# Kernel optimization log

Hardware: AMD Instinct MI355X
Metric: run time of the kernel (lower is better)

## Reference

```python
import jax, jax.numpy as jnp
import numpy as np

B, LV, LS = 16, 512, 512
FEA_V, FEA_S = 2048, 768
D_MODEL, H, DK, DV = 1024, 16, 64, 64
EPS = 1e-6


def setup_inputs() -> dict:
    key = jax.random.key(0)
    ks = jax.random.split(key, 16)
    sc = lambda fan_in: 1.0 / np.sqrt(fan_in)
    return {
        "v": jax.random.normal(ks[0], (B, LV, FEA_V), jnp.float32),
        "s": jax.random.normal(ks[1], (B, LS, FEA_S), jnp.float32),
        "W_lv": jax.random.normal(ks[2], (FEA_V, D_MODEL), jnp.float32) * sc(FEA_V),
        "b_lv": jnp.zeros((D_MODEL,), jnp.float32),
        "W_ls": jax.random.normal(ks[3], (FEA_S, D_MODEL), jnp.float32) * sc(FEA_S),
        "b_ls": jnp.zeros((D_MODEL,), jnp.float32),
        "pos_v": jax.random.normal(ks[4], (1, LV, D_MODEL), jnp.float32),
        "pos_s": jax.random.normal(ks[5], (1, LS, D_MODEL), jnp.float32),
        "W_q": jax.random.normal(ks[6], (D_MODEL, H * DK), jnp.float32) * sc(D_MODEL),
        "b_q": jnp.zeros((H * DK,), jnp.float32),
        "W_k": jax.random.normal(ks[7], (D_MODEL, H * DK), jnp.float32) * sc(D_MODEL),
        "b_k": jnp.zeros((H * DK,), jnp.float32),
        "W_v": jax.random.normal(ks[8], (D_MODEL, H * DV), jnp.float32) * sc(D_MODEL),
        "b_v": jnp.zeros((H * DV,), jnp.float32),
        "W_p": jax.random.normal(ks[9], (H * DV, D_MODEL), jnp.float32) * sc(H * DV),
        "b_p": jnp.zeros((D_MODEL,), jnp.float32),
        "ln_gamma": jnp.ones((D_MODEL,), jnp.float32),
        "ln_beta": jnp.zeros((D_MODEL,), jnp.float32),
        "v_len": LV,
        "s_len": LS,
    }


def _layer_norm(x, gamma, beta):
    mu = jnp.mean(x, axis=-1, keepdims=True)
    var = jnp.var(x, axis=-1, keepdims=True)
    return gamma * (x - mu) / jnp.sqrt(var + EPS) + beta


def reference(v, s, W_lv, b_lv, W_ls, b_ls, pos_v, pos_s, W_q, b_q, W_k, b_k,
              W_v, b_v, W_p, b_p, ln_gamma, ln_beta, v_len, s_len):
    b_size = v.shape[0]
    # input projections + ReLU (dropout is identity at eval)
    v = jax.nn.relu(v @ W_lv + b_lv)  # [B, LV, D]
    s = jax.nn.relu(s @ W_ls + b_ls)  # [B, LS, D]
    # positional embedding add (pos=True)
    residual_v = v + pos_v[:, : v.shape[1], :]
    # QKV projections; note the original unpack `q_v, k_s, k_s = ...`
    # overwrites the key with the VALUE projection of s, so both key and
    # value in attention are v_s (the W_v projection of s). W_k output is
    # computed in torch but discarded.
    q = (v @ W_q + b_q).reshape(b_size, -1, H, DK).transpose(0, 2, 1, 3)   # [B,H,LV,DK]
    _k = (s @ W_k + b_k)  # computed then discarded, kept for faithfulness
    vs = (s @ W_v + b_v).reshape(b_size, -1, H, DV).transpose(0, 2, 1, 3)  # [B,H,LS,DV]
    scores = jnp.einsum("bhqd,bhkd->bhqk", q, vs) / jnp.sqrt(jnp.float32(DK))
    attn = jax.nn.softmax(scores, axis=-1)
    context = jnp.einsum("bhqk,bhkd->bhqd", attn, vs)  # [B,H,LV,DV]
    context = context.transpose(0, 2, 1, 3).reshape(b_size, -1, H * DV)
    output_v = context @ W_p + b_p  # dropout identity at eval
    return _layer_norm(residual_v + output_v, ln_gamma, ln_beta)
```

## Files before the change

kernel.cpp:

```cpp
#include <hip/hip_runtime.h>

typedef unsigned short u16;
typedef unsigned int   u32;

using bf16x8 = __attribute__((ext_vector_type(8))) short;
using f32x4  = __attribute__((ext_vector_type(4))) float;

#define MFMA16(a, b, c) __builtin_amdgcn_mfma_f32_16x16x32_bf16((a), (b), (c), 0, 0, 0)

__device__ __forceinline__ u16 f2bf(float f) {
  union { float f; u32 u; } x; x.f = f;
  u32 r = x.u + 0x7fffu + ((x.u >> 16) & 1u);
  return (u16)(r >> 16);
}

__device__ __forceinline__ float bf2f(u16 v) {
  union { u32 u; float f; } x; x.u = ((u32)v) << 16;
  return x.f;
}

__device__ __forceinline__ u32 cvtpk(float lo, float hi) {
  u32 r;
  asm("v_cvt_pk_bf16_f32 %0, %1, %2" : "=v"(r) : "v"(lo), "v"(hi));
  return r;
}

__device__ __forceinline__ void gl2lds16(const void* g, void* l) {
  __builtin_amdgcn_global_load_lds(
      (const __attribute__((address_space(1))) u32*)g,
      (__attribute__((address_space(3))) u32*)l, 16, 0, 0);
}

__global__ __launch_bounds__(256) void cvt_f32_bf16(const float* __restrict__ in,
                                                    u16* __restrict__ out, long n8) {
  long i = (long)blockIdx.x * 256 + threadIdx.x;
  if (i >= n8) return;
  const float4* p = (const float4*)(in + i * 8);
  float4 a = p[0], b = p[1];
  uint4 pk;
  pk.x = cvtpk(a.x, a.y);
  pk.y = cvtpk(a.z, a.w);
  pk.z = cvtpk(b.x, b.y);
  pk.w = cvtpk(b.z, b.w);
  *(uint4*)(out + i * 8) = pk;
}

__global__ __launch_bounds__(256) void wt_cvt_t(const float* __restrict__ W,
                                                u16* __restrict__ Wt, int K, int N) {
  __shared__ u16 t[64][66];
  int tilesN = N >> 6;
  int k0 = ((int)blockIdx.x / tilesN) << 6;
  int n0 = ((int)blockIdx.x % tilesN) << 6;
  int tid = threadIdx.x;
  int c4 = (tid & 15) * 4, r16 = tid >> 4;
#pragma unroll
  for (int p = 0; p < 4; ++p) {
    int row = r16 + p * 16;
    float4 f = *(const float4*)(W + (size_t)(k0 + row) * N + n0 + c4);
    t[row][c4 + 0] = f2bf(f.x);
    t[row][c4 + 1] = f2bf(f.y);
    t[row][c4 + 2] = f2bf(f.z);
    t[row][c4 + 3] = f2bf(f.w);
  }
  __syncthreads();
  int c8 = (tid & 7) * 8, r32 = tid >> 3;
#pragma unroll
  for (int p = 0; p < 2; ++p) {
    int n = r32 + p * 32;
    u16 tmp[8] __attribute__((aligned(16)));
#pragma unroll
    for (int e = 0; e < 8; ++e) tmp[e] = t[c8 + e][n];
    *(uint4*)(Wt + (size_t)(n0 + n) * K + k0 + c8) = *(uint4*)tmp;
  }
}

template <int MODE>
__global__ __launch_bounds__(512) void gemm_bf16(
    const u16* __restrict__ A, const u16* __restrict__ Bt,
    const float* __restrict__ bias, u16* __restrict__ outb, float* __restrict__ outf,
    u16* __restrict__ outt, const u16* __restrict__ add0b,
    const float* __restrict__ add1, int M, int N, int K) {
  __shared__ u16 sA[2][128 * 64];
  __shared__ u16 sB[2][128 * 64];
  int tilesN = N >> 7;
  int nwg = (int)gridDim.x;
  int cpx = nwg >> 3;
  int orig = (int)blockIdx.x;
  int wg = (orig & 7) * cpx + (orig >> 3);
  int tm = wg / tilesN, tn = wg % tilesN;
  int m0 = tm << 7, n0 = tn << 7;
  int tid = threadIdx.x, w = tid >> 6, l = tid & 63;
  int wm = (w >> 2) << 6, wn = (w & 3) << 5;
  int c16 = l & 15, hi = l >> 4, g16 = hi * 16;

  f32x4 acc[4][2];
#pragma unroll
  for (int i = 0; i < 4; ++i)
#pragma unroll
    for (int j = 0; j < 2; ++j) acc[i][j] = (f32x4){0.f, 0.f, 0.f, 0.f};

  auto STAGE = [&](int kt, int buf) {
    const u16* Ab = A + (size_t)m0 * K + kt * 64;
    const u16* Bb = Bt + (size_t)n0 * K + kt * 64;
#pragma unroll
    for (int p = 0; p < 2; ++p) {
      int lin = p * 8192 + tid * 16;
      int row = lin >> 7;
      int cb = (lin & 127) ^ ((row & 7) << 4);
      int base = lin & ~1023;
      gl2lds16(Ab + (size_t)row * K + (cb >> 1), (char*)sA[buf] + base);
      gl2lds16(Bb + (size_t)row * K + (cb >> 1), (char*)sB[buf] + base);
    }
  };

  auto COMPUTE = [&](int buf) {
#pragma unroll
    for (int kk = 0; kk < 2; ++kk) {
      bf16x8 af[4], bfr[2];
#pragma unroll
      for (int i = 0; i < 4; ++i) {
        int ar = wm + i * 16 + c16;
        af[i] = *(const bf16x8*)((const char*)sA[buf] + ar * 128 +
                                 ((kk * 64 + g16) ^ ((ar & 7) << 4)));
      }
#pragma unroll
      for (int j = 0; j < 2; ++j) {
        int br = wn + j * 16 + c16;
        bfr[j] = *(const bf16x8*)((const char*)sB[buf] + br * 128 +
                                  ((kk * 64 + g16) ^ ((br & 7) << 4)));
      }
#pragma unroll
      for (int i = 0; i < 4; ++i)
#pragma unroll
        for (int j = 0; j < 2; ++j) acc[i][j] = MFMA16(bfr[j], af[i], acc[i][j]);
    }
  };

  int nk = K >> 6;
  STAGE(0, 0);
  int cur = 0;
  for (int kt = 0; kt < nk; ++kt) {
    if (kt + 1 < nk) {
      STAGE(kt + 1, cur ^ 1);
      __builtin_amdgcn_sched_barrier(0);
      asm volatile("s_waitcnt vmcnt(4)" ::: "memory");
    } else {
      asm volatile("s_waitcnt vmcnt(0)" ::: "memory");
    }
    __builtin_amdgcn_s_barrier();
    __builtin_amdgcn_sched_barrier(0);
    COMPUTE(cur);
    __builtin_amdgcn_sched_barrier(0);
    __builtin_amdgcn_s_barrier();
    cur ^= 1;
  }

#pragma unroll
  for (int i = 0; i < 4; ++i) {
    int gm = m0 + wm + i * 16 + c16;
#pragma unroll
    for (int j = 0; j < 2; ++j) {
      int gn0 = n0 + wn + j * 16 + hi * 4;
      float4 b4 = *(const float4*)(bias + gn0);
      float vv[4];
      vv[0] = acc[i][j][0] + b4.x;
      vv[1] = acc[i][j][1] + b4.y;
      vv[2] = acc[i][j][2] + b4.z;
      vv[3] = acc[i][j][3] + b4.w;
      if (MODE == 0) {
#pragma unroll
        for (int r = 0; r < 4; ++r) vv[r] = fmaxf(vv[r], 0.f);
        uint2 pw;
        pw.x = cvtpk(vv[0], vv[1]);
        pw.y = cvtpk(vv[2], vv[3]);
        *(uint2*)(outb + (size_t)gm * N + gn0) = pw;
      } else if (MODE == 2 || MODE == 4) {
        int hh = gn0 >> 6, dk0 = gn0 & 63, bb2 = gm >> 9, ll2 = gm & 511;
        uint2 pw;
        pw.x = cvtpk(vv[0], vv[1]);
        pw.y = cvtpk(vv[2], vv[3]);
        *(uint2*)(outb + (((size_t)bb2 * 16 + hh) * 512 + ll2) * 64 + dk0) = pw;
        if (MODE == 4) {
          u16* tb = outt + ((size_t)bb2 * 16 + hh) * 32768 + ll2;
#pragma unroll
          for (int r = 0; r < 4; ++r) tb[(size_t)(dk0 + r) * 512] = f2bf(vv[r]);
        }
      } else {
        uint2 a0 = *(const uint2*)(add0b + (size_t)gm * N + gn0);
        float4 a1 = *(const float4*)(add1 + (size_t)(gm & 511) * N + gn0);
        float4 o;
        o.x = vv[0] + bf2f((u16)(a0.x & 0xffff)) + a1.x;
        o.y = vv[1] + bf2f((u16)(a0.x >> 16)) + a1.y;
        o.z = vv[2] + bf2f((u16)(a0.y & 0xffff)) + a1.z;
        o.w = vv[3] + bf2f((u16)(a0.y >> 16)) + a1.w;
        *(float4*)(outf + (size_t)gm * N + gn0) = o;
      }
    }
  }
}

__global__ __launch_bounds__(512) void attn_kernel(const u16* __restrict__ q,
                                                   const u16* __restrict__ kv,
                                                   const u16* __restrict__ kvT,
                                                   u16* __restrict__ ctx) {
  __shared__ u16 sK[2][4096];
  __shared__ u16 sVT[2][4096];
  __shared__ u16 sP[8192];

  int orig = (int)blockIdx.x;
  int r = (orig & 7) * 128 + (orig >> 3);
  int bh = r >> 2, qt = r & 3;
  int b = bh >> 4, h = bh & 15;
  int tid = threadIdx.x, w = tid >> 6, l = tid & 63;
  int c16 = l & 15, hi = l >> 4, g16 = hi * 16;
  int swzq = (c16 & 7) << 4;

  const u16* qbase = q + (size_t)bh * 32768 + (size_t)qt * 8192;
#pragma unroll
  for (int j = 0; j < 2; ++j) {
    int chunk = w * 2 + j;
    int lin = chunk * 1024 + l * 16;
    int row = lin >> 7;
    int cb = (lin & 127) ^ ((row & 7) << 4);
    gl2lds16(qbase + (size_t)row * 64 + (cb >> 1), (char*)sP + chunk * 1024);
  }
  {
    const u16* kb = kv + (size_t)bh * 32768;
    const u16* vb = kvT + (size_t)bh * 32768;
    int lin = w * 1024 + l * 16;
    int row = lin >> 7;
    int cb = (lin & 127) ^ ((row & 7) << 4);
    gl2lds16(kb + (size_t)row * 64 + (cb >> 1), (char*)sK[0] + w * 1024);
    gl2lds16(vb + (size_t)row * 512 + (cb >> 1), (char*)sVT[0] + w * 1024);
  }
  __syncthreads();

  const char* sQrow = (const char*)sP + (w * 16 + c16) * 128;
  bf16x8 qf0 = *(const bf16x8*)(sQrow + ((0 + g16) ^ swzq));
  bf16x8 qf1 = *(const bf16x8*)(sQrow + ((64 + g16) ^ swzq));

  char* sPw = (char*)sP + w * 2048;
  f32x4 of[4];
#pragma unroll
  for (int n = 0; n < 4; ++n) of[n] = (f32x4){0.f, 0.f, 0.f, 0.f};
  float m_run = -1e30f, l_run = 0.f;

  for (int c = 0; c < 8; ++c) {
    int cur = c & 1;
    if (c < 7) {
      const u16* kb = kv + (size_t)bh * 32768 + (size_t)(c + 1) * 4096;
      const u16* vb = kvT + (size_t)bh * 32768 + (c + 1) * 64;
      int lin = w * 1024 + l * 16;
      int row = lin >> 7;
      int cb = (lin & 127) ^ ((row & 7) << 4);
      gl2lds16(kb + (size_t)row * 64 + (cb >> 1), (char*)sK[cur ^ 1] + w * 1024);
      gl2lds16(vb + (size_t)row * 512 + (cb >> 1), (char*)sVT[cur ^ 1] + w * 1024);
    }
    const char* kbuf = (const char*)sK[cur];
    const char* vtbuf = (const char*)sVT[cur];

    f32x4 sf[4];
#pragma unroll
    for (int n = 0; n < 4; ++n) {
      const char* krow = kbuf + (n * 16 + c16) * 128;
      bf16x8 k0 = *(const bf16x8*)(krow + (g16 ^ swzq));
      bf16x8 k1 = *(const bf16x8*)(krow + ((64 + g16) ^ swzq));
      f32x4 z = (f32x4){0.f, 0.f, 0.f, 0.f};
      z = MFMA16(k0, qf0, z);
      z = MFMA16(k1, qf1, z);
      sf[n] = z;
    }

    float pmax = -1e30f;
#pragma unroll
    for (int n = 0; n < 4; ++n)
#pragma unroll
      for (int rr = 0; rr < 4; ++rr) {
        sf[n][rr] *= 0.125f;
        pmax = fmaxf(pmax, sf[n][rr]);
      }
    pmax = fmaxf(pmax, __shfl_xor(pmax, 16));
    pmax = fmaxf(pmax, __shfl_xor(pmax, 32));
    float mnew = fmaxf(m_run, pmax);
    float corr = __expf(m_run - mnew);
    float psum = 0.f;
#pragma unroll
    for (int n = 0; n < 4; ++n)
#pragma unroll
      for (int rr = 0; rr < 4; ++rr) {
        float p = __expf(sf[n][rr] - mnew);
        sf[n][rr] = p;
        psum += p;
      }
    psum += __shfl_xor(psum, 16);
    psum += __shfl_xor(psum, 32);
    l_run = l_run * corr + psum;
    m_run = mnew;
#pragma unroll
    for (int n = 0; n < 4; ++n)
#pragma unroll
      for (int rr = 0; rr < 4; ++rr) of[n][rr] *= corr;

#pragma unroll
    for (int n = 0; n < 4; ++n) {
      uint2 pw;
      pw.x = cvtpk(sf[n][0], sf[n][1]);
      pw.y = cvtpk(sf[n][2], sf[n][3]);
      *(uint2*)(sPw + c16 * 128 + ((n * 32 + hi * 8) ^ swzq)) = pw;
    }

    bf16x8 pf0 = *(const bf16x8*)(sPw + c16 * 128 + (g16 ^ swzq));
    bf16x8 pf1 = *(const bf16x8*)(sPw + c16 * 128 + ((64 + g16) ^ swzq));
#pragma unroll
    for (int n = 0; n < 4; ++n) {
      const char* vrow = vtbuf + (n * 16 + c16) * 128;
      bf16x8 v0 = *(const bf16x8*)(vrow + (g16 ^ swzq));
      bf16x8 v1 = *(const bf16x8*)(vrow + ((64 + g16) ^ swzq));
      of[n] = MFMA16(v0, pf0, of[n]);
      of[n] = MFMA16(v1, pf1, of[n]);
    }
    __syncthreads();
  }

  float inv = 1.0f / l_run;
  int grow = qt * 128 + w * 16 + c16;
  u16* obase = ctx + (size_t)(b * 512 + grow) * 1024 + h * 64;
#pragma unroll
  for (int n = 0; n < 4; ++n) {
    uint2 ow;
    ow.x = cvtpk(of[n][0] * inv, of[n][1] * inv);
    ow.y = cvtpk(of[n][2] * inv, of[n][3] * inv);
    *(uint2*)(obase + n * 16 + hi * 4) = ow;
  }
}

__global__ __launch_bounds__(256) void ln_kernel(float* __restrict__ x,
                                                 const float* __restrict__ gamma,
                                                 const float* __restrict__ beta) {
  __shared__ float red[4];
  __shared__ float red2[4];
  int row = blockIdx.x, tid = threadIdx.x;
  float4 v = *(float4*)(x + (size_t)row * 1024 + tid * 4);
  float s = v.x + v.y + v.z + v.w;
#pragma unroll
  for (int d = 1; d < 64; d <<= 1) s += __shfl_xor(s, d);
  if ((tid & 63) == 0) red[tid >> 6] = s;
  __syncthreads();
  float mu = (red[0] + red[1] + red[2] + red[3]) * (1.0f / 1024.0f);
  float d0 = v.x - mu, d1 = v.y - mu, d2 = v.z - mu, d3 = v.w - mu;
  float qq = d0 * d0 + d1 * d1 + d2 * d2 + d3 * d3;
#pragma unroll
  for (int d = 1; d < 64; d <<= 1) qq += __shfl_xor(qq, d);
  if ((tid & 63) == 0) red2[tid >> 6] = qq;
  __syncthreads();
  float var = (red2[0] + red2[1] + red2[2] + red2[3]) * (1.0f / 1024.0f);
  float rstd = rsqrtf(var + 1e-6f);
  float4 g = *(const float4*)(gamma + tid * 4);
  float4 bb = *(const float4*)(beta + tid * 4);
  v.x = g.x * d0 * rstd + bb.x;
  v.y = g.y * d1 * rstd + bb.y;
  v.z = g.z * d2 * rstd + bb.z;
  v.w = g.w * d3 * rstd + bb.w;
  *(float4*)(x + (size_t)row * 1024 + tid * 4) = v;
}

extern "C" void kernel_launch(void* const* d_in, const int* in_sizes, int n_in,
                              void* d_out, int out_size, void* d_ws, size_t ws_size,
                              hipStream_t stream) {
  (void)in_sizes; (void)n_in; (void)out_size; (void)ws_size;
  const float* v_in  = (const float*)d_in[0];
  const float* s_in  = (const float*)d_in[1];
  const float* W_lv  = (const float*)d_in[2];
  const float* b_lv  = (const float*)d_in[3];
  const float* W_ls  = (const float*)d_in[4];
  const float* b_ls  = (const float*)d_in[5];
  const float* pos_v = (const float*)d_in[6];
  const float* W_q   = (const float*)d_in[8];
  const float* b_q   = (const float*)d_in[9];
  const float* W_v   = (const float*)d_in[12];
  const float* b_v   = (const float*)d_in[13];
  const float* W_p   = (const float*)d_in[14];
  const float* b_p   = (const float*)d_in[15];
  const float* gamma = (const float*)d_in[16];
  const float* beta  = (const float*)d_in[17];
  float* out = (float*)d_out;

  char* ws = (char*)d_ws;
  size_t off = 0;
  auto alloc = [&](size_t bytes) {
    char* p = ws + off;
    off += (bytes + 255) & ~(size_t)255;
    return p;
  };
  u16* v_bf     = (u16*)alloc(33554432);
  u16* s_bf     = (u16*)alloc(12582912);
  u16* Wlv_t    = (u16*)alloc(4194304);
  u16* Wls_t    = (u16*)alloc(1572864);
  u16* Wq_t     = (u16*)alloc(2097152);
  u16* Wv_t     = (u16*)alloc(2097152);
  u16* Wp_t     = (u16*)alloc(2097152);
  u16* vproj_bf = (u16*)alloc(16777216);
  u16* sproj_bf = (u16*)alloc(16777216);
  u16* q_bf     = (u16*)alloc(16777216);
  u16* vs_bf    = (u16*)alloc(16777216);
  u16* vsT_bf   = (u16*)alloc(16777216);
  u16* ctx_bf   = (u16*)alloc(16777216);

  cvt_f32_bf16<<<8192, 256, 0, stream>>>(v_in, v_bf, 2097152);
  cvt_f32_bf16<<<3072, 256, 0, stream>>>(s_in, s_bf, 786432);
  wt_cvt_t<<<512, 256, 0, stream>>>(W_lv, Wlv_t, 2048, 1024);
  wt_cvt_t<<<192, 256, 0, stream>>>(W_ls, Wls_t, 768, 1024);
  wt_cvt_t<<<256, 256, 0, stream>>>(W_q, Wq_t, 1024, 1024);
  wt_cvt_t<<<256, 256, 0, stream>>>(W_v, Wv_t, 1024, 1024);
  wt_cvt_t<<<256, 256, 0, stream>>>(W_p, Wp_t, 1024, 1024);

  gemm_bf16<0><<<512, 512, 0, stream>>>(v_bf, Wlv_t, b_lv, vproj_bf, nullptr,
                                        nullptr, nullptr, nullptr, 8192, 1024, 2048);
  gemm_bf16<0><<<512, 512, 0, stream>>>(s_bf, Wls_t, b_ls, sproj_bf, nullptr,
                                        nullptr, nullptr, nullptr, 8192, 1024, 768);
  gemm_bf16<2><<<512, 512, 0, stream>>>(vproj_bf, Wq_t, b_q, q_bf, nullptr,
                                        nullptr, nullptr, nullptr, 8192, 1024, 1024);
  gemm_bf16<4><<<512, 512, 0, stream>>>(sproj_bf, Wv_t, b_v, vs_bf, nullptr,
                                        vsT_bf, nullptr, nullptr, 8192, 1024, 1024);
  attn_kernel<<<1024, 512, 0, stream>>>(q_bf, vs_bf, vsT_bf, ctx_bf);
  gemm_bf16<3><<<512, 512, 0, stream>>>(ctx_bf, Wp_t, b_p, nullptr, out,
                                        nullptr, vproj_bf, pos_v, 8192, 1024, 1024);
  ln_kernel<<<8192, 256, 0, stream>>>(out, gamma, beta);
}
```

Before: 231.0 us.

## Fuse fp32-to-bf16 activation conversion into input projection GEMM A-tile loading

Removes the separate conversion kernels for v and s. The input-projection GEMMs now read fp32 activations directly, convert them to bf16 in registers and write the swizzled tiles into LDS. A register-staged prefetch pipeline replaces the direct global-to-LDS path for A. This removes the bf16 intermediate write and read and two launches, but each A tile is now re-read as fp32 by every column-tile block, and register pressure goes up.

```diff
diff --git a/kernel.cpp b/kernel.cpp
--- a/kernel.cpp
+++ b/kernel.cpp
@@ -29,20 +29,6 @@
   __builtin_amdgcn_global_load_lds(
       (const __attribute__((address_space(1))) u32*)g,
       (__attribute__((address_space(3))) u32*)l, 16, 0, 0);
-}
-
-__global__ __launch_bounds__(256) void cvt_f32_bf16(const float* __restrict__ in,
-                                                    u16* __restrict__ out, long n8) {
-  long i = (long)blockIdx.x * 256 + threadIdx.x;
-  if (i >= n8) return;
-  const float4* p = (const float4*)(in + i * 8);
-  float4 a = p[0], b = p[1];
-  uint4 pk;
-  pk.x = cvtpk(a.x, a.y);
-  pk.y = cvtpk(a.z, a.w);
-  pk.z = cvtpk(b.x, b.y);
-  pk.w = cvtpk(b.z, b.w);
-  *(uint4*)(out + i * 8) = pk;
 }
 
 __global__ __launch_bounds__(256) void wt_cvt_t(const float* __restrict__ W,
@@ -74,9 +60,9 @@
   }
 }
 
-template <int MODE>
+template <int MODE, bool AF32>
 __global__ __launch_bounds__(512) void gemm_bf16(
-    const u16* __restrict__ A, const u16* __restrict__ Bt,
+    const void* __restrict__ Av, const u16* __restrict__ Bt,
     const float* __restrict__ bias, u16* __restrict__ outb, float* __restrict__ outf,
     u16* __restrict__ outt, const u16* __restrict__ add0b,
     const float* __restrict__ add1, int M, int N, int K) {
@@ -99,20 +85,6 @@
 #pragma unroll
     for (int j = 0; j < 2; ++j) acc[i][j] = (f32x4){0.f, 0.f, 0.f, 0.f};
 
-  auto STAGE = [&](int kt, int buf) {
-    const u16* Ab = A + (size_t)m0 * K + kt * 64;
-    const u16* Bb = Bt + (size_t)n0 * K + kt * 64;
-#pragma unroll
-    for (int p = 0; p < 2; ++p) {
-      int lin = p * 8192 + tid * 16;
-      int row = lin >> 7;
-      int cb = (lin & 127) ^ ((row & 7) << 4);
-      int base = lin & ~1023;
-      gl2lds16(Ab + (size_t)row * K + (cb >> 1), (char*)sA[buf] + base);
-      gl2lds16(Bb + (size_t)row * K + (cb >> 1), (char*)sB[buf] + base);
-    }
-  };
-
   auto COMPUTE = [&](int buf) {
 #pragma unroll
     for (int kk = 0; kk < 2; ++kk) {
@@ -137,22 +109,106 @@
   };
 
   int nk = K >> 6;
-  STAGE(0, 0);
-  int cur = 0;
-  for (int kt = 0; kt < nk; ++kt) {
-    if (kt + 1 < nk) {
-      STAGE(kt + 1, cur ^ 1);
+
+  if constexpr (!AF32) {
+    const u16* A = (const u16*)Av;
+    auto STAGE = [&](int kt, int buf) {
+      const u16* Ab = A + (size_t)m0 * K + kt * 64;
+      const u16* Bb = Bt + (size_t)n0 * K + kt * 64;
+#pragma unroll
+      for (int p = 0; p < 2; ++p) {
+        int lin = p * 8192 + tid * 16;
+        int row = lin >> 7;
+        int cb = (lin & 127) ^ ((row & 7) << 4);
+        int base = lin & ~1023;
+        gl2lds16(Ab + (size_t)row * K + (cb >> 1), (char*)sA[buf] + base);
+        gl2lds16(Bb + (size_t)row * K + (cb >> 1), (char*)sB[buf] + base);
+      }
+    };
+    STAGE(0, 0);
+    int cur = 0;
+    for (int kt = 0; kt < nk; ++kt) {
+      if (kt + 1 < nk) {
+        STAGE(kt + 1, cur ^ 1);
+        __builtin_amdgcn_sched_barrier(0);
+        asm volatile("s_waitcnt vmcnt(4)" ::: "memory");
+      } else {
+        asm volatile("s_waitcnt vmcnt(0)" ::: "memory");
+      }
+      __builtin_amdgcn_s_barrier();
       __builtin_amdgcn_sched_barrier(0);
-      asm volatile("s_waitcnt vmcnt(4)" ::: "memory");
-    } else {
-      asm volatile("s_waitcnt vmcnt(0)" ::: "memory");
-    }
+      COMPUTE(cur);
+      __builtin_amdgcn_sched_barrier(0);
+      __builtin_amdgcn_s_barrier();
+      cur ^= 1;
+    }
+  } else {
+    const float* Af = (const float*)Av;
+    int arow = tid >> 2;
+    int acol = (tid & 3) * 32;
+    int aswz = (arow & 7) << 4;
+    float4 fr0, fr1, fr2, fr3;
+    auto AF_ISSUE = [&](int kt) {
+      const float* s = Af + (size_t)(m0 + arow) * K + kt * 64 + (acol >> 1);
+      fr0 = *(const float4*)(s + 0);
+      fr1 = *(const float4*)(s + 4);
+      fr2 = *(const float4*)(s + 8);
+      fr3 = *(const float4*)(s + 12);
+    };
+    auto AF_WRITE = [&](int buf) {
+      uint4 w0, w1;
+      w0.x = cvtpk(fr0.x, fr0.y); w0.y = cvtpk(fr0.z, fr0.w);
+      w0.z = cvtpk(fr1.x, fr1.y); w0.w = cvtpk(fr1.z, fr1.w);
+      w1.x = cvtpk(fr2.x, fr2.y); w1.y = cvtpk(fr2.z, fr2.w);
+      w1.z = cvtpk(fr3.x, fr3.y); w1.w = cvtpk(fr3.z, fr3.w);
+      char* base = (char*)sA[buf] + arow * 128;
+      *(uint4*)(base + (acol ^ aswz)) = w0;
+      *(uint4*)(base + ((acol + 16) ^ aswz)) = w1;
+    };
+    auto STAGE_B = [&](int kt, int buf) {
+      const u16* Bb = Bt + (size_t)n0 * K + kt * 64;
+#pragma unroll
+      for (int p = 0; p < 2; ++p) {
+        int lin = p * 8192 + tid * 16;
+        int row = lin >> 7;
+        int cb = (lin & 127) ^ ((row & 7) << 4);
+        gl2lds16(Bb + (size_t)row * K + (cb >> 1), (char*)sB[buf] + (lin & ~1023));
+      }
+    };
+
+    AF_ISSUE(0);
+    asm volatile("s_waitcnt vmcnt(0)" ::: "memory");
+    AF_WRITE(0);
+    AF_ISSUE(1);
+    STAGE_B(0, 0);
+    __builtin_amdgcn_sched_barrier(0);
+    asm volatile("s_waitcnt lgkmcnt(0)" ::: "memory");
     __builtin_amdgcn_s_barrier();
-    __builtin_amdgcn_sched_barrier(0);
-    COMPUTE(cur);
-    __builtin_amdgcn_sched_barrier(0);
-    __builtin_amdgcn_s_barrier();
-    cur ^= 1;
+
+    int cur = 0;
+    for (int kt = 0; kt < nk; ++kt) {
+      if (kt + 1 < nk) {
+        asm volatile("s_waitcnt vmcnt(2)" ::: "memory");
+        __builtin_amdgcn_sched_barrier(0);
+        AF_WRITE(cur ^ 1);
+        if (kt + 2 < nk) AF_ISSUE(kt + 2);
+        STAGE_B(kt + 1, cur ^ 1);
+        __builtin_amdgcn_sched_barrier(0);
+        if (kt + 2 < nk)
+          asm volatile("s_waitcnt vmcnt(6)" ::: "memory");
+        else
+          asm volatile("s_waitcnt vmcnt(2)" ::: "memory");
+      } else {
+        asm volatile("s_waitcnt vmcnt(0)" ::: "memory");
+      }
+      __builtin_amdgcn_s_barrier();
+      __builtin_amdgcn_sched_barrier(0);
+      COMPUTE(cur);
+      __builtin_amdgcn_sched_barrier(0);
+      asm volatile("s_waitcnt lgkmcnt(0)" ::: "memory");
+      __builtin_amdgcn_s_barrier();
+      cur ^= 1;
+    }
   }
 
 #pragma unroll
@@ -392,8 +448,6 @@
     off += (bytes + 255) & ~(size_t)255;
     return p;
   };
-  u16* v_bf     = (u16*)alloc(33554432);
-  u16* s_bf     = (u16*)alloc(12582912);
   u16* Wlv_t    = (u16*)alloc(4194304);
   u16* Wls_t    = (u16*)alloc(1572864);
   u16* Wq_t     = (u16*)alloc(2097152);
@@ -406,24 +460,22 @@
   u16* vsT_bf   = (u16*)alloc(16777216);
   u16* ctx_bf   = (u16*)alloc(16777216);
 
-  cvt_f32_bf16<<<8192, 256, 0, stream>>>(v_in, v_bf, 2097152);
-  cvt_f32_bf16<<<3072, 256, 0, stream>>>(s_in, s_bf, 786432);
   wt_cvt_t<<<512, 256, 0, stream>>>(W_lv, Wlv_t, 2048, 1024);
   wt_cvt_t<<<192, 256, 0, stream>>>(W_ls, Wls_t, 768, 1024);
   wt_cvt_t<<<256, 256, 0, stream>>>(W_q, Wq_t, 1024, 1024);
   wt_cvt_t<<<256, 256, 0, stream>>>(W_v, Wv_t, 1024, 1024);
   wt_cvt_t<<<256, 256, 0, stream>>>(W_p, Wp_t, 1024, 1024);
 
-  gemm_bf16<0><<<512, 512, 0, stream>>>(v_bf, Wlv_t, b_lv, vproj_bf, nullptr,
-                                        nullptr, nullptr, nullptr, 8192, 1024, 2048);
-  gemm_bf16<0><<<512, 512, 0, stream>>>(s_bf, Wls_t, b_ls, sproj_bf, nullptr,
-                                        nullptr, nullptr, nullptr, 8192, 1024, 768);
-  gemm_bf16<2><<<512, 512, 0, stream>>>(vproj_bf, Wq_t, b_q, q_bf, nullptr,
-                                        nullptr, nullptr, nullptr, 8192, 1024, 1024);
-  gemm_bf16<4><<<512, 512, 0, stream>>>(sproj_bf, Wv_t, b_v, vs_bf, nullptr,
-                                        vsT_bf, nullptr, nullptr, 8192, 1024, 1024);
+  gemm_bf16<0, true><<<512, 512, 0, stream>>>(v_in, Wlv_t, b_lv, vproj_bf, nullptr,
+                                              nullptr, nullptr, nullptr, 8192, 1024, 2048);
+  gemm_bf16<0, true><<<512, 512, 0, stream>>>(s_in, Wls_t, b_ls, sproj_bf, nullptr,
+                                              nullptr, nullptr, nullptr, 8192, 1024, 768);
+  gemm_bf16<2, false><<<512, 512, 0, stream>>>(vproj_bf, Wq_t, b_q, q_bf, nullptr,
+                                               nullptr, nullptr, nullptr, 8192, 1024, 1024);
+  gemm_bf16<4, false><<<512, 512, 0, stream>>>(sproj_bf, Wv_t, b_v, vs_bf, nullptr,
+                                               vsT_bf, nullptr, nullptr, 8192, 1024, 1024);
   attn_kernel<<<1024, 512, 0, stream>>>(q_bf, vs_bf, vsT_bf, ctx_bf);
-  gemm_bf16<3><<<512, 512, 0, stream>>>(ctx_bf, Wp_t, b_p, nullptr, out,
-                                        nullptr, vproj_bf, pos_v, 8192, 1024, 1024);
+  gemm_bf16<3, false><<<512, 512, 0, stream>>>(ctx_bf, Wp_t, b_p, nullptr, out,
+                                               nullptr, vproj_bf, pos_v, 8192, 1024, 1024);
   ln_kernel<<<8192, 256, 0, stream>>>(out, gamma, beta);
 }
```

Result: slower. 244.3 us (+5.7%).
